# Performance work log

Measured on AMD Instinct MI355X. Metric: run time of the kernel, lower is better.

Reference implementation:

```python
import jax, jax.numpy as jnp
import numpy as np

T, S, B, H, NH, F = 256, 128, 32, 1024, 16, 4096
D = H // NH  # head dim


def setup_inputs() -> dict:
    key = jax.random.key(0)
    ks = jax.random.split(key, 14)
    w = lambda k, shape: jax.random.normal(k, shape, jnp.float32) * 0.02
    return {
        "x": jax.random.normal(ks[0], (T, B, H), jnp.float32),
        "src_bias": jnp.zeros((B, 1, 1, S), jnp.float32),
        "tgt_bias": jnp.zeros((B, 1, 1, T), jnp.float32),
        "memory": jax.random.normal(ks[1], (S, B, H), jnp.float32),
        # cross-attention projections
        "Wq": w(ks[2], (H, H)), "bq": jnp.zeros((H,), jnp.float32),
        "Wk": w(ks[3], (H, H)), "bk": jnp.zeros((H,), jnp.float32),
        "Wv": w(ks[4], (H, H)), "bv": jnp.zeros((H,), jnp.float32),
        "Wo": w(ks[5], (H, H)), "bo": jnp.zeros((H,), jnp.float32),
        # feed-forward
        "W1": w(ks[6], (H, F)), "b1": jnp.zeros((F,), jnp.float32),
        "W2": w(ks[7], (F, H)), "b2": jnp.zeros((H,), jnp.float32),
        # LSTM gates: input = cat(ffn_x, attn_ctx, h) -> 3H, output 4H (i,j,f,o)
        "Wg": w(ks[8], (3 * H, 4 * H)), "bg": jnp.zeros((4 * H,), jnp.float32),
    }


def _cross_attention(xq, mem, bias, Wq, bq, Wk, bk, Wv, bv, Wo, bo):
    # xq: [B,T,H], mem: [B,S,H], bias: [B,1,1,S]
    b, t, h = xq.shape
    q = (xq @ Wq + bq).reshape(b, t, NH, D) * (D ** -0.5)
    k = (mem @ Wk + bk).reshape(b, -1, NH, D)
    v = (mem @ Wv + bv).reshape(b, -1, NH, D)
    logits = jnp.einsum("bqhd,bkhd->bhqk", q, k) + bias
    wts = jax.nn.softmax(logits, axis=-1)
    ctx = jnp.einsum("bhqk,bkhd->bqhd", wts, v).reshape(b, t, h)
    return ctx @ Wo + bo


def reference(x, src_bias, tgt_bias, memory, Wq, bq, Wk, bk, Wv, bv, Wo, bo,
              W1, b1, W2, b2, Wg, bg):
    # cross attention (time-major -> batch-major -> time-major)
    c_attn = _cross_attention(jnp.transpose(x, (1, 0, 2)),
                              jnp.transpose(memory, (1, 0, 2)),
                              src_bias, Wq, bq, Wk, bk, Wv, bv, Wo, bo)
    c_attn = jnp.transpose(c_attn, (1, 0, 2))  # [T,B,H]

    # feed-forward on x (dropout disabled / eval mode)
    ffn_x = jax.nn.relu(x @ W1 + b1) @ W2 + b2  # [T,B,H]

    xs = jnp.concatenate([ffn_x, c_attn], axis=-1)  # [T,B,2H]
    c0 = jnp.zeros((x.shape[1], H), x.dtype)
    h0 = jnp.zeros((x.shape[1], H), x.dtype)

    def step(carry, xt):
        c, h = carry
        g = jnp.concatenate([xt, h], axis=-1) @ Wg + bg  # [B,4H]
        i = jax.nn.sigmoid(g[:, :H])
        j = jnp.tanh(g[:, H:2 * H])
        f = jax.nn.sigmoid(g[:, 2 * H:3 * H])
        o = jax.nn.sigmoid(g[:, 3 * H:])
        new_c = f * c + i * j
        new_h = o * new_c  # THUMT LSTMCell default activation=None
        return (new_c, new_h), new_h

    (c_f, h_f), hiddens = jax.lax.scan(step, (c0, h0), xs)
    return hiddens, c_f, h_f
```

## Files before the change

### kernel.cpp

```cpp
#include <hip/hip_runtime.h>
#include <cstdint>
#include <cstddef>

#define T_  256
#define S_  128
#define B_  32
#define H_  1024
#define NH_ 16
#define D_  64
#define F_  4096
#define TB_ (T_*B_)
#define SB_ (S_*B_)

typedef unsigned short u16;
typedef unsigned int   u32;
typedef unsigned long long u64;
typedef __attribute__((ext_vector_type(8))) short s16x8;
typedef __attribute__((ext_vector_type(4))) float f32x4;
typedef __attribute__((ext_vector_type(4))) u32  u32x4;

static __device__ __forceinline__ float b2f(u16 u) {
  union { u32 i; float f; } cv; cv.i = ((u32)u) << 16; return cv.f;
}
static __device__ __forceinline__ u16 f2b(float f) {
  union { float f; u32 i; } cv; cv.f = f;
  u32 u = cv.i;
  u32 r = (u + 0x7fffu + ((u >> 16) & 1u)) >> 16;
  return (u16)r;
}
static __device__ __forceinline__ float sigm(float x) {
  return 1.0f / (1.0f + __expf(-x));
}
static __device__ __forceinline__ float tanh_fast(float x) {
  float e2 = __expf(2.0f * x);
  return 1.0f - 2.0f / (e2 + 1.0f);
}

typedef const __attribute__((address_space(1))) void* gvoidp;
typedef __attribute__((address_space(3))) void* lvoidp;
static __device__ __forceinline__ void gl_lds16(const void* g, void* l) {
  __builtin_amdgcn_global_load_lds((gvoidp)g, (lvoidp)l, 16, 0, 0);
}

__global__ void cast_bf16(const float* __restrict__ in, u16* __restrict__ out, int n4) {
  int i = blockIdx.x * 256 + threadIdx.x;
  if (i < n4) {
    float4 v = reinterpret_cast<const float4*>(in)[i];
    ushort4 o;
    o.x = f2b(v.x); o.y = f2b(v.y); o.z = f2b(v.z); o.w = f2b(v.w);
    reinterpret_cast<ushort4*>(out)[i] = o;
  }
}

__global__ void transpose_cast(const float* __restrict__ in, u16* __restrict__ out,
                               int R, int C) {
  __shared__ float tile[32][33];
  int c0 = blockIdx.x * 32, r0 = blockIdx.y * 32;
  int tx = threadIdx.x, ty = threadIdx.y;
  #pragma unroll
  for (int k = 0; k < 32; k += 8)
    tile[ty + k][tx] = in[(size_t)(r0 + ty + k) * C + c0 + tx];
  __syncthreads();
  #pragma unroll
  for (int k = 0; k < 32; k += 8)
    out[(size_t)(c0 + ty + k) * R + r0 + tx] = f2b(tile[tx][ty + k]);
}

__global__ void rearrange_wh(const u16* __restrict__ WhT, u16* __restrict__ WhR) {
  int idx = blockIdx.x * 256 + threadIdx.x;
  int lane = idx & 63;
  int kc = (idx >> 6) & 7;
  int g  = (idx >> 9) & 3;
  int w  = (idx >> 11) & 3;
  int bk = idx >> 13;
  int row = g * H_ + bk * 16 + (lane & 15);
  int col = w * 256 + kc * 32 + (lane >> 4) * 8;
  *(uint4*)&WhR[(size_t)idx * 8] = *(const uint4*)&WhT[(size_t)row * H_ + col];
}

__global__ __launch_bounds__(256) void gemm_bt(
    const u16* __restrict__ A, const u16* __restrict__ Bt,
    u16* __restrict__ Out, const float* __restrict__ bias,
    int Kdim, int ostride, float scale, int relu)
{
  __shared__ __align__(16) u16 As[128 * 32];
  __shared__ __align__(16) u16 Bs[128 * 32];
  const int tid  = threadIdx.x;
  const int wave = tid >> 6, lane = tid & 63;
  const int quad = lane >> 4, l16 = lane & 15;
  const int bm = blockIdx.y << 7, bn = blockIdx.x << 7;
  const int wm = (wave & 1) << 6, wn = (wave >> 1) << 6;
  f32x4 acc[4][4] = {};

  const int sr = wave * 32 + (lane >> 2);
  const int sc = (lane & 3) * 8;
  const u16* ga = &A [(size_t)(bm + sr) * Kdim + sc];
  const u16* gb = &Bt[(size_t)(bn + sr) * Kdim + sc];
  u16* lA = &As[wave * 1024];
  u16* lB = &Bs[wave * 1024];
  const size_t rowskip = (size_t)16 * Kdim;

  for (int k0 = 0; k0 < Kdim; k0 += 32) {
    gl_lds16(ga + k0,           lA);
    gl_lds16(ga + k0 + rowskip, lA + 512);
    gl_lds16(gb + k0,           lB);
    gl_lds16(gb + k0 + rowskip, lB + 512);
    __syncthreads();
    s16x8 af[4], bf[4];
    #pragma unroll
    for (int mt = 0; mt < 4; mt++)
      af[mt] = *(const s16x8*)&As[(wm + mt * 16 + l16) * 32 + quad * 8];
    #pragma unroll
    for (int nt = 0; nt < 4; nt++)
      bf[nt] = *(const s16x8*)&Bs[(wn + nt * 16 + l16) * 32 + quad * 8];
    #pragma unroll
    for (int mt = 0; mt < 4; mt++)
      #pragma unroll
      for (int nt = 0; nt < 4; nt++)
        acc[mt][nt] = __builtin_amdgcn_mfma_f32_16x16x32_bf16(af[mt], bf[nt], acc[mt][nt], 0, 0, 0);
    __syncthreads();
  }

  #pragma unroll
  for (int mt = 0; mt < 4; mt++) {
    #pragma unroll
    for (int nt = 0; nt < 4; nt++) {
      const int col = bn + wn + nt * 16 + l16;
      const float bv = bias[col];
      #pragma unroll
      for (int r = 0; r < 4; r++) {
        const int row = bm + wm + mt * 16 + quad * 4 + r;
        float vv = (acc[mt][nt][r] + bv) * scale;
        if (relu) vv = fmaxf(vv, 0.0f);
        Out[(size_t)row * ostride + col] = f2b(vv);
      }
    }
  }
}

__global__ __launch_bounds__(256) void attn_kernel(
    const u16* __restrict__ q, const u16* __restrict__ k, const u16* __restrict__ v,
    const float* __restrict__ src_bias, u16* __restrict__ ctx)
{
  __shared__ u16 ks[S_ * D_];
  __shared__ u16 vs[S_ * D_];
  const int b  = blockIdx.x >> 4;
  const int nh = blockIdx.x & 15;
  const int tid = threadIdx.x;

  for (int i = tid; i < (S_ * D_) / 8; i += 256) {
    int s = i >> 3, c = (i & 7) * 8;
    *(uint4*)&ks[s * D_ + c] = *(const uint4*)&k[((size_t)(s * B_ + b)) * H_ + nh * D_ + c];
    *(uint4*)&vs[s * D_ + c] = *(const uint4*)&v[((size_t)(s * B_ + b)) * H_ + nh * D_ + c];
  }
  __syncthreads();

  const int t = tid;
  float qf[D_];
  const u16* qp = &q[((size_t)(t * B_ + b)) * H_ + nh * D_];
  #pragma unroll
  for (int c8 = 0; c8 < D_; c8 += 8) {
    uint4 qv = *(const uint4*)&qp[c8];
    const u16* pu = (const u16*)&qv;
    #pragma unroll
    for (int j = 0; j < 8; j++) qf[c8 + j] = b2f(pu[j]);
  }
  const float* bias = src_bias + b * S_;

  float m = -1e30f, l = 0.0f;
  for (int s = 0; s < S_; s++) {
    float dot = 0.0f;
    #pragma unroll
    for (int d = 0; d < D_; d++) dot += qf[d] * b2f(ks[s * D_ + d]);
    dot += bias[s];
    float nm = fmaxf(m, dot);
    l = l * __expf(m - nm) + __expf(dot - nm);
    m = nm;
  }
  float of[D_] = {};
  const float inv = 1.0f / l;
  for (int s = 0; s < S_; s++) {
    float dot = 0.0f;
    #pragma unroll
    for (int d = 0; d < D_; d++) dot += qf[d] * b2f(ks[s * D_ + d]);
    dot += bias[s];
    float w = __expf(dot - m) * inv;
    #pragma unroll
    for (int d = 0; d < D_; d++) of[d] += w * b2f(vs[s * D_ + d]);
  }
  u16* op = &ctx[((size_t)(t * B_ + b)) * H_ + nh * D_];
  #pragma unroll
  for (int c8 = 0; c8 < D_; c8 += 8) {
    u16 tmp[8];
    #pragma unroll
    for (int j = 0; j < 8; j++) tmp[j] = f2b(of[c8 + j]);
    *(uint4*)&op[c8] = *(const uint4*)tmp;
  }
}

#define ISSUE2(K) { \
  const u16* b0_ = hb + ((size_t)(wave * 16 + (K) * 2 + (quad >> 1))) * 512 + \
                   (quad & 1) * 8 + l16 * 16; \
  asm volatile("global_load_dwordx4 %0, %1, off sc0 sc1" : "=v"(ba[K][0]) : "v"(b0_) : "memory"); \
  asm volatile("global_load_dwordx4 %0, %1, off sc0 sc1" : "=v"(ba[K][1]) : "v"(b0_ + 256) : "memory"); }

#define DO_MFMA(A0,A1,KC)                                                           \
  { _Pragma("unroll") for (int g_ = 0; g_ < 3; g_++) {                              \
      s16x8 wf_ = *(const s16x8*)&Wl[wave][((g_ * 8 + (KC)) * 64 + lane) * 8];      \
      acc[g_][0] = __builtin_amdgcn_mfma_f32_16x16x32_bf16(A0, wf_, acc[g_][0], 0, 0, 0); \
      acc[g_][1] = __builtin_amdgcn_mfma_f32_16x16x32_bf16(A1, wf_, acc[g_][1], 0, 0, 0); } \
    acc[3][0] = __builtin_amdgcn_mfma_f32_16x16x32_bf16(A0, wo[KC], acc[3][0], 0, 0, 0);  \
    acc[3][1] = __builtin_amdgcn_mfma_f32_16x16x32_bf16(A1, wo[KC], acc[3][1], 0, 0, 0); }

#define CONSUME(K, NSTR) { \
  asm volatile("s_waitcnt vmcnt(" NSTR ")" ::: "memory"); \
  __builtin_amdgcn_sched_barrier(0); \
  DO_MFMA(ba[K][0], ba[K][1], K); }

__global__ __launch_bounds__(256, 1) void lstm_persistent(
    const u16* __restrict__ g_x, const u16* __restrict__ WhR,
    u16* __restrict__ hb16, u32* __restrict__ sent, float* __restrict__ out)
{
  __shared__ __align__(16) u16 Wl[4][3 * 8 * 64 * 8];
  __shared__ float P[4][4][32][17];
  const int bk = blockIdx.x, tid = threadIdx.x;
  const int wave = tid >> 6, lane = tid & 63;
  const int quad = lane >> 4, l16 = lane & 15;

  const u16* wsrc = WhR + ((size_t)(bk * 4 + wave) * 4 * 8 * 64) * 8;
  for (int i = lane; i < 3 * 8 * 64; i += 64)
    *(uint4*)&Wl[wave][i * 8] = *(const uint4*)&wsrc[(size_t)i * 8];
  s16x8 wo[8];
  #pragma unroll
  for (int kc = 0; kc < 8; kc++)
    wo[kc] = *(const s16x8*)&wsrc[((size_t)(3 * 8 + kc) * 64 + lane) * 8];
  __syncthreads();

  const int pb = tid >> 4, pc = tid & 15;
  const int col = bk * 16 + pc;
  float creg[2] = {0.0f, 0.0f};

  float gxp[2][4];
  #pragma unroll
  for (int ii = 0; ii < 2; ii++)
    #pragma unroll
    for (int g = 0; g < 4; g++)
      gxp[ii][g] = b2f(g_x[((size_t)(pb + ii * 16)) * (4 * H_) + g * H_ + col]);

  s16x8 ba[8][2];

  for (int t = 0; t < T_; t++) {
    if (t > 0) {
      const u32 st = (u32)t;
      const u16* hb = hb16 + ((t & 1) ^ 1) * 32768;

      { const u32* sp = sent + ((size_t)(((t & 1) ^ 1) * 256 + wave * 64 + lane));
        u32 sv;
        do {
          asm volatile("global_load_dword %0, %1, off sc0 sc1\n\ts_waitcnt vmcnt(0)"
                       : "=v"(sv) : "v"(sp) : "memory");
        } while (!__all(sv == st)); }

      f32x4 acc[4][2] = {};
      ISSUE2(0) ISSUE2(1) ISSUE2(2) ISSUE2(3)
      ISSUE2(4) ISSUE2(5) ISSUE2(6) ISSUE2(7)
      CONSUME(0, "14") CONSUME(1, "12") CONSUME(2, "10") CONSUME(3, "8")
      CONSUME(4, "6")  CONSUME(5, "4")  CONSUME(6, "2")  CONSUME(7, "0")

      #pragma unroll
      for (int g = 0; g < 4; g++)
        #pragma unroll
        for (int mt = 0; mt < 2; mt++)
          #pragma unroll
          for (int r = 0; r < 4; r++)
            P[wave][g][mt * 16 + quad * 4 + r][l16] = acc[g][mt][r];
    }
    __syncthreads();

    float gs[2][4];
    #pragma unroll
    for (int ii = 0; ii < 2; ii++) {
      const int b_ = pb + ii * 16;
      #pragma unroll
      for (int g = 0; g < 4; g++) {
        float s = gxp[ii][g];
        if (t > 0) s += P[0][g][b_][pc] + P[1][g][b_][pc] + P[2][g][b_][pc] + P[3][g][b_][pc];
        gs[ii][g] = s;
      }
    }
    __syncthreads();

    float hn[2], cn[2];
    #pragma unroll
    for (int ii = 0; ii < 2; ii++) {
      const float iv = sigm(gs[ii][0]);
      const float jv = tanh_fast(gs[ii][1]);
      const float fv = sigm(gs[ii][2]);
      const float ov = sigm(gs[ii][3]);
      cn[ii] = fv * creg[ii] + iv * jv;
      hn[ii] = ov * cn[ii];
      creg[ii] = cn[ii];
    }

    {
      u32 lo0 = f2b(hn[0]), lo1 = f2b(hn[1]);
      u32 hi0 = __shfl_down(lo0, 1), hi1 = __shfl_down(lo1, 1);
      if ((pc & 1) == 0) {
        u32* hw32 = (u32*)(hb16 + (t & 1) * 32768);
        u32 dw0 = lo0 | (hi0 << 16);
        u32 dw1 = lo1 | (hi1 << 16);
        __hip_atomic_store(&hw32[(size_t)bk * 256 + pb * 8 + (pc >> 1)], dw0,
                           __ATOMIC_RELAXED, __HIP_MEMORY_SCOPE_AGENT);
        __hip_atomic_store(&hw32[(size_t)bk * 256 + (pb + 16) * 8 + (pc >> 1)], dw1,
                           __ATOMIC_RELAXED, __HIP_MEMORY_SCOPE_AGENT);
      }
      asm volatile("s_waitcnt vmcnt(0)" ::: "memory");
      if (lane == 0)
        __hip_atomic_store(&sent[(size_t)(t & 1) * 256 + bk * 4 + wave], (u32)(t + 1),
                           __ATOMIC_RELAXED, __HIP_MEMORY_SCOPE_AGENT);
    }

    #pragma unroll
    for (int ii = 0; ii < 2; ii++) {
      const int b_ = pb + ii * 16;
      out[(size_t)t * (B_ * H_) + b_ * H_ + col] = hn[ii];
      if (t == T_ - 1) {
        out[(size_t)T_ * B_ * H_ + b_ * H_ + col] = cn[ii];
        out[(size_t)T_ * B_ * H_ + B_ * H_ + b_ * H_ + col] = hn[ii];
      }
    }
    if (t < T_ - 1) {
      #pragma unroll
      for (int ii = 0; ii < 2; ii++)
        #pragma unroll
        for (int g = 0; g < 4; g++)
          gxp[ii][g] = b2f(g_x[((size_t)(t + 1) * B_ + pb + ii * 16) * (4 * H_) + g * H_ + col]);
    }
  }
}

extern "C" void kernel_launch(void* const* d_in, const int* in_sizes, int n_in,
                              void* d_out, int out_size, void* d_ws, size_t ws_size,
                              hipStream_t stream)
{
  const float* x        = (const float*)d_in[0];
  const float* src_bias = (const float*)d_in[1];
  const float* mem      = (const float*)d_in[3];
  const float* Wq = (const float*)d_in[4];  const float* bq = (const float*)d_in[5];
  const float* Wk = (const float*)d_in[6];  const float* bk = (const float*)d_in[7];
  const float* Wv = (const float*)d_in[8];  const float* bv = (const float*)d_in[9];
  const float* Wo = (const float*)d_in[10]; const float* bo = (const float*)d_in[11];
  const float* W1 = (const float*)d_in[12]; const float* b1 = (const float*)d_in[13];
  const float* W2 = (const float*)d_in[14]; const float* b2 = (const float*)d_in[15];
  const float* Wg = (const float*)d_in[16]; const float* bg = (const float*)d_in[17];
  float* out = (float*)d_out;

  char* p = (char*)d_ws;
  u16* xb   = (u16*)p; p += (size_t)TB_ * H_ * 2;
  u16* memb = (u16*)p; p += (size_t)SB_ * H_ * 2;
  u16* WqT  = (u16*)p; p += (size_t)H_ * H_ * 2;
  u16* WkT  = (u16*)p; p += (size_t)H_ * H_ * 2;
  u16* WvT  = (u16*)p; p += (size_t)H_ * H_ * 2;
  u16* WoT  = (u16*)p; p += (size_t)H_ * H_ * 2;
  u16* W1T  = (u16*)p; p += (size_t)F_ * H_ * 2;
  u16* W2T  = (u16*)p; p += (size_t)H_ * F_ * 2;
  u16* WgxT = (u16*)p; p += (size_t)(4 * H_) * (2 * H_) * 2;
  u16* WhT  = (u16*)p; p += (size_t)(4 * H_) * H_ * 2;
  u16* WhR  = (u16*)p; p += (size_t)(4 * H_) * H_ * 2;
  u16* qb   = (u16*)p; p += (size_t)TB_ * H_ * 2;
  u16* kb   = (u16*)p; p += (size_t)SB_ * H_ * 2;
  u16* vb   = (u16*)p; p += (size_t)SB_ * H_ * 2;
  u16* ctxb = (u16*)p; p += (size_t)TB_ * H_ * 2;
  u16* xs   = (u16*)p; p += (size_t)TB_ * (2 * H_) * 2;
  u16* h1   = (u16*)p; p += (size_t)TB_ * F_ * 2;
  u16* hb16 = (u16*)p; p += (size_t)2 * 32768 * 2;
  u32* sent = (u32*)p; p += (size_t)2 * 256 * 4;
  u16* gx   = h1;

  hipMemsetAsync(sent, 0, 2 * 256 * 4, stream);

  cast_bf16<<<dim3((TB_ * H_ / 4) / 256), dim3(256), 0, stream>>>(x, xb, TB_ * H_ / 4);
  cast_bf16<<<dim3((SB_ * H_ / 4) / 256), dim3(256), 0, stream>>>(mem, memb, SB_ * H_ / 4);

  dim3 tb(32, 8);
  transpose_cast<<<dim3(H_ / 32, H_ / 32), tb, 0, stream>>>(Wq, WqT, H_, H_);
  transpose_cast<<<dim3(H_ / 32, H_ / 32), tb, 0, stream>>>(Wk, WkT, H_, H_);
  transpose_cast<<<dim3(H_ / 32, H_ / 32), tb, 0, stream>>>(Wv, WvT, H_, H_);
  transpose_cast<<<dim3(H_ / 32, H_ / 32), tb, 0, stream>>>(Wo, WoT, H_, H_);
  transpose_cast<<<dim3(F_ / 32, H_ / 32), tb, 0, stream>>>(W1, W1T, H_, F_);
  transpose_cast<<<dim3(H_ / 32, F_ / 32), tb, 0, stream>>>(W2, W2T, F_, H_);
  transpose_cast<<<dim3(4 * H_ / 32, 2 * H_ / 32), tb, 0, stream>>>(Wg, WgxT, 2 * H_, 4 * H_);
  transpose_cast<<<dim3(4 * H_ / 32, H_ / 32), tb, 0, stream>>>(Wg + (size_t)(2 * H_) * (4 * H_), WhT, H_, 4 * H_);
  rearrange_wh<<<dim3(2048), 256, 0, stream>>>(WhT, WhR);

  gemm_bt<<<dim3(H_ / 128, TB_ / 128), 256, 0, stream>>>(xb, WqT, qb, bq, H_, H_, 0.125f, 0);
  gemm_bt<<<dim3(H_ / 128, SB_ / 128), 256, 0, stream>>>(memb, WkT, kb, bk, H_, H_, 1.0f, 0);
  gemm_bt<<<dim3(H_ / 128, SB_ / 128), 256, 0, stream>>>(memb, WvT, vb, bv, H_, H_, 1.0f, 0);

  attn_kernel<<<dim3(B_ * NH_), 256, 0, stream>>>(qb, kb, vb, src_bias, ctxb);

  gemm_bt<<<dim3(H_ / 128, TB_ / 128), 256, 0, stream>>>(ctxb, WoT, xs + H_, bo, H_, 2 * H_, 1.0f, 0);

  gemm_bt<<<dim3(F_ / 128, TB_ / 128), 256, 0, stream>>>(xb, W1T, h1, b1, H_, F_, 1.0f, 1);
  gemm_bt<<<dim3(H_ / 128, TB_ / 128), 256, 0, stream>>>(h1, W2T, xs, b2, F_, 2 * H_, 1.0f, 0);

  gemm_bt<<<dim3(4 * H_ / 128, TB_ / 128), 256, 0, stream>>>(xs, WgxT, gx, bg, 2 * H_, 4 * H_, 1.0f, 0);

  lstm_persistent<<<dim3(64), 256, 0, stream>>>(gx, WhR, hb16, sent, out);
}
```

Before: 1.774 ms.

## Merge prep kernels and batch independent GEMMs into grouped launches

```diff
diff --git a/kernel.cpp b/kernel.cpp
--- a/kernel.cpp
+++ b/kernel.cpp
@@ -42,21 +42,23 @@
   __builtin_amdgcn_global_load_lds((gvoidp)g, (lvoidp)l, 16, 0, 0);
 }
 
-__global__ void cast_bf16(const float* __restrict__ in, u16* __restrict__ out, int n4) {
-  int i = blockIdx.x * 256 + threadIdx.x;
-  if (i < n4) {
-    float4 v = reinterpret_cast<const float4*>(in)[i];
-    ushort4 o;
-    o.x = f2b(v.x); o.y = f2b(v.y); o.z = f2b(v.z); o.w = f2b(v.w);
-    reinterpret_cast<ushort4*>(out)[i] = o;
-  }
-}
-
-__global__ void transpose_cast(const float* __restrict__ in, u16* __restrict__ out,
-                               int R, int C) {
-  __shared__ float tile[32][33];
-  int c0 = blockIdx.x * 32, r0 = blockIdx.y * 32;
-  int tx = threadIdx.x, ty = threadIdx.y;
+static __device__ __forceinline__ void cast_task(const float* __restrict__ in,
+                                                 u16* __restrict__ out, int lb, int tid) {
+  int i = lb * 256 + tid;
+  float4 v = reinterpret_cast<const float4*>(in)[i];
+  ushort4 o;
+  o.x = f2b(v.x); o.y = f2b(v.y); o.z = f2b(v.z); o.w = f2b(v.w);
+  reinterpret_cast<ushort4*>(out)[i] = o;
+}
+
+static __device__ __forceinline__ void tr32(const float* __restrict__ in,
+                                            u16* __restrict__ out,
+                                            int R, int C, int lin, int tid,
+                                            float tile[32][33]) {
+  const int gx = C >> 5;
+  const int bx = lin % gx, by = lin / gx;
+  const int c0 = bx << 5, r0 = by << 5;
+  const int tx = tid & 31, ty = tid >> 5;
   #pragma unroll
   for (int k = 0; k < 32; k += 8)
     tile[ty + k][tx] = in[(size_t)(r0 + ty + k) * C + c0 + tx];
@@ -66,29 +68,54 @@
     out[(size_t)(c0 + ty + k) * R + r0 + tx] = f2b(tile[tx][ty + k]);
 }
 
-__global__ void rearrange_wh(const u16* __restrict__ WhT, u16* __restrict__ WhR) {
-  int idx = blockIdx.x * 256 + threadIdx.x;
-  int lane = idx & 63;
-  int kc = (idx >> 6) & 7;
-  int g  = (idx >> 9) & 3;
-  int w  = (idx >> 11) & 3;
-  int bk = idx >> 13;
-  int row = g * H_ + bk * 16 + (lane & 15);
-  int col = w * 256 + kc * 32 + (lane >> 4) * 8;
-  *(uint4*)&WhR[(size_t)idx * 8] = *(const uint4*)&WhT[(size_t)row * H_ + col];
-}
-
-__global__ __launch_bounds__(256) void gemm_bt(
+#define NB_SENT 1
+#define NB_CX   8192
+#define NB_CM   4096
+#define NB_TSQ  1024
+#define NB_TW1  4096
+#define NB_TW2  4096
+#define NB_TGX  8192
+#define NB_TWH  4096
+#define NB_PREP (NB_SENT + NB_CX + NB_CM + 4*NB_TSQ + NB_TW1 + NB_TW2 + NB_TGX + NB_TWH)
+
+__global__ __launch_bounds__(256) void prep_all(
+    const float* __restrict__ x, const float* __restrict__ mem,
+    const float* __restrict__ Wq, const float* __restrict__ Wk,
+    const float* __restrict__ Wv, const float* __restrict__ Wo,
+    const float* __restrict__ W1, const float* __restrict__ W2,
+    const float* __restrict__ Wg,
+    u16* __restrict__ xb, u16* __restrict__ memb,
+    u16* __restrict__ WqT, u16* __restrict__ WkT, u16* __restrict__ WvT,
+    u16* __restrict__ WoT, u16* __restrict__ W1T, u16* __restrict__ W2T,
+    u16* __restrict__ WgxT, u16* __restrict__ WhT, u32* __restrict__ sent)
+{
+  __shared__ float tile[32][33];
+  int b = blockIdx.x;
+  const int tid = threadIdx.x;
+  if (b < NB_SENT) { sent[tid] = 0; sent[tid + 256] = 0; return; }
+  b -= NB_SENT;
+  if (b < NB_CX) { cast_task(x, xb, b, tid); return; }      b -= NB_CX;
+  if (b < NB_CM) { cast_task(mem, memb, b, tid); return; }  b -= NB_CM;
+  if (b < NB_TSQ) { tr32(Wq, WqT, H_, H_, b, tid, tile); return; }  b -= NB_TSQ;
+  if (b < NB_TSQ) { tr32(Wk, WkT, H_, H_, b, tid, tile); return; }  b -= NB_TSQ;
+  if (b < NB_TSQ) { tr32(Wv, WvT, H_, H_, b, tid, tile); return; }  b -= NB_TSQ;
+  if (b < NB_TSQ) { tr32(Wo, WoT, H_, H_, b, tid, tile); return; }  b -= NB_TSQ;
+  if (b < NB_TW1) { tr32(W1, W1T, H_, F_, b, tid, tile); return; }  b -= NB_TW1;
+  if (b < NB_TW2) { tr32(W2, W2T, F_, H_, b, tid, tile); return; }  b -= NB_TW2;
+  if (b < NB_TGX) { tr32(Wg, WgxT, 2 * H_, 4 * H_, b, tid, tile); return; } b -= NB_TGX;
+  tr32(Wg + (size_t)(2 * H_) * (4 * H_), WhT, H_, 4 * H_, b, tid, tile);
+}
+
+static __device__ __forceinline__ void gemm_core(
     const u16* __restrict__ A, const u16* __restrict__ Bt,
     u16* __restrict__ Out, const float* __restrict__ bias,
-    int Kdim, int ostride, float scale, int relu)
-{
-  __shared__ __align__(16) u16 As[128 * 32];
-  __shared__ __align__(16) u16 Bs[128 * 32];
+    int Kdim, int ostride, float scale, int relu,
+    int bx, int by, u16* As, u16* Bs)
+{
   const int tid  = threadIdx.x;
   const int wave = tid >> 6, lane = tid & 63;
   const int quad = lane >> 4, l16 = lane & 15;
-  const int bm = blockIdx.y << 7, bn = blockIdx.x << 7;
+  const int bm = by << 7, bn = bx << 7;
   const int wm = (wave & 1) << 6, wn = (wave >> 1) << 6;
   f32x4 acc[4][4] = {};
 
@@ -138,6 +165,28 @@
   }
 }
 
+struct GJob {
+  const u16* A; const u16* Bt; u16* Out; const float* bias;
+  int Kdim; int ostride; int relu; int gridx; int nblk; float scale;
+};
+struct GBatch { GJob j[4]; int starts[4]; int njobs; };
+
+__global__ __launch_bounds__(256) void gemm_multi(GBatch gb)
+{
+  __shared__ __align__(16) u16 As[128 * 32];
+  __shared__ __align__(16) u16 Bs[128 * 32];
+  const int bid = blockIdx.x;
+  int ji = 0;
+  #pragma unroll
+  for (int t = 1; t < 4; t++)
+    if (t < gb.njobs && bid >= gb.starts[t]) ji = t;
+  const GJob J = gb.j[ji];
+  const int lin = bid - gb.starts[ji];
+  const int wg = (lin & 7) * (J.nblk >> 3) + (lin >> 3);
+  const int bx = wg % J.gridx, by = wg / J.gridx;
+  gemm_core(J.A, J.Bt, J.Out, J.bias, J.Kdim, J.ostride, J.scale, J.relu, bx, by, As, Bs);
+}
+
 __global__ __launch_bounds__(256) void attn_kernel(
     const u16* __restrict__ q, const u16* __restrict__ k, const u16* __restrict__ v,
     const float* __restrict__ src_bias, u16* __restrict__ ctx)
@@ -218,7 +267,7 @@
   DO_MFMA(ba[K][0], ba[K][1], K); }
 
 __global__ __launch_bounds__(256, 1) void lstm_persistent(
-    const u16* __restrict__ g_x, const u16* __restrict__ WhR,
+    const u16* __restrict__ g_x, const u16* __restrict__ WhT,
     u16* __restrict__ hb16, u32* __restrict__ sent, float* __restrict__ out)
 {
   __shared__ __align__(16) u16 Wl[4][3 * 8 * 64 * 8];
@@ -227,13 +276,21 @@
   const int wave = tid >> 6, lane = tid & 63;
   const int quad = lane >> 4, l16 = lane & 15;
 
-  const u16* wsrc = WhR + ((size_t)(bk * 4 + wave) * 4 * 8 * 64) * 8;
-  for (int i = lane; i < 3 * 8 * 64; i += 64)
-    *(uint4*)&Wl[wave][i * 8] = *(const uint4*)&wsrc[(size_t)i * 8];
+  for (int i = lane; i < 3 * 8 * 64; i += 64) {
+    const int g  = (i >> 9) & 3;
+    const int kc = (i >> 6) & 7;
+    const int row = g * H_ + bk * 16 + (lane & 15);
+    const int col = wave * 256 + kc * 32 + (lane >> 4) * 8;
+    *(uint4*)&Wl[wave][i * 8] = *(const uint4*)&WhT[(size_t)row * H_ + col];
+  }
   s16x8 wo[8];
-  #pragma unroll
-  for (int kc = 0; kc < 8; kc++)
-    wo[kc] = *(const s16x8*)&wsrc[((size_t)(3 * 8 + kc) * 64 + lane) * 8];
+  {
+    const int row = 3 * H_ + bk * 16 + (lane & 15);
+    const int colb = wave * 256 + (lane >> 4) * 8;
+    #pragma unroll
+    for (int kc = 0; kc < 8; kc++)
+      wo[kc] = *(const s16x8*)&WhT[(size_t)row * H_ + colb + kc * 32];
+  }
   __syncthreads();
 
   const int pb = tid >> 4, pc = tid & 15;
@@ -350,8 +407,8 @@
   const float* Wk = (const float*)d_in[6];  const float* bk = (const float*)d_in[7];
   const float* Wv = (const float*)d_in[8];  const float* bv = (const float*)d_in[9];
   const float* Wo = (const float*)d_in[10]; const float* bo = (const float*)d_in[11];
-  const float* W1 = (const float*)d_in[12]; const float* b1 = (const float*)d_in[13];
-  const float* W2 = (const float*)d_in[14]; const float* b2 = (const float*)d_in[15];
+  const float* W1 = (const float*)d_in[12]; const float* b1f = (const float*)d_in[13];
+  const float* W2 = (const float*)d_in[14]; const float* b2f_ = (const float*)d_in[15];
   const float* Wg = (const float*)d_in[16]; const float* bg = (const float*)d_in[17];
   float* out = (float*)d_out;
 
@@ -366,7 +423,6 @@
   u16* W2T  = (u16*)p; p += (size_t)H_ * F_ * 2;
   u16* WgxT = (u16*)p; p += (size_t)(4 * H_) * (2 * H_) * 2;
   u16* WhT  = (u16*)p; p += (size_t)(4 * H_) * H_ * 2;
-  u16* WhR  = (u16*)p; p += (size_t)(4 * H_) * H_ * 2;
   u16* qb   = (u16*)p; p += (size_t)TB_ * H_ * 2;
   u16* kb   = (u16*)p; p += (size_t)SB_ * H_ * 2;
   u16* vb   = (u16*)p; p += (size_t)SB_ * H_ * 2;
@@ -377,34 +433,39 @@
   u32* sent = (u32*)p; p += (size_t)2 * 256 * 4;
   u16* gx   = h1;
 
-  hipMemsetAsync(sent, 0, 2 * 256 * 4, stream);
-
-  cast_bf16<<<dim3((TB_ * H_ / 4) / 256), dim3(256), 0, stream>>>(x, xb, TB_ * H_ / 4);
-  cast_bf16<<<dim3((SB_ * H_ / 4) / 256), dim3(256), 0, stream>>>(mem, memb, SB_ * H_ / 4);
-
-  dim3 tb(32, 8);
-  transpose_cast<<<dim3(H_ / 32, H_ / 32), tb, 0, stream>>>(Wq, WqT, H_, H_);
-  transpose_cast<<<dim3(H_ / 32, H_ / 32), tb, 0, stream>>>(Wk, WkT, H_, H_);
-  transpose_cast<<<dim3(H_ / 32, H_ / 32), tb, 0, stream>>>(Wv, WvT, H_, H_);
-  transpose_cast<<<dim3(H_ / 32, H_ / 32), tb, 0, stream>>>(Wo, WoT, H_, H_);
-  transpose_cast<<<dim3(F_ / 32, H_ / 32), tb, 0, stream>>>(W1, W1T, H_, F_);
-  transpose_cast<<<dim3(H_ / 32, F_ / 32), tb, 0, stream>>>(W2, W2T, F_, H_);
-  transpose_cast<<<dim3(4 * H_ / 32, 2 * H_ / 32), tb, 0, stream>>>(Wg, WgxT, 2 * H_, 4 * H_);
-  transpose_cast<<<dim3(4 * H_ / 32, H_ / 32), tb, 0, stream>>>(Wg + (size_t)(2 * H_) * (4 * H_), WhT, H_, 4 * H_);
-  rearrange_wh<<<dim3(2048), 256, 0, stream>>>(WhT, WhR);
-
-  gemm_bt<<<dim3(H_ / 128, TB_ / 128), 256, 0, stream>>>(xb, WqT, qb, bq, H_, H_, 0.125f, 0);
-  gemm_bt<<<dim3(H_ / 128, SB_ / 128), 256, 0, stream>>>(memb, WkT, kb, bk, H_, H_, 1.0f, 0);
-  gemm_bt<<<dim3(H_ / 128, SB_ / 128), 256, 0, stream>>>(memb, WvT, vb, bv, H_, H_, 1.0f, 0);
-
-  attn_kernel<<<dim3(B_ * NH_), 256, 0, stream>>>(qb, kb, vb, src_bias, ctxb);
-
-  gemm_bt<<<dim3(H_ / 128, TB_ / 128), 256, 0, stream>>>(ctxb, WoT, xs + H_, bo, H_, 2 * H_, 1.0f, 0);
-
-  gemm_bt<<<dim3(F_ / 128, TB_ / 128), 256, 0, stream>>>(xb, W1T, h1, b1, H_, F_, 1.0f, 1);
-  gemm_bt<<<dim3(H_ / 128, TB_ / 128), 256, 0, stream>>>(h1, W2T, xs, b2, F_, 2 * H_, 1.0f, 0);
-
-  gemm_bt<<<dim3(4 * H_ / 128, TB_ / 128), 256, 0, stream>>>(xs, WgxT, gx, bg, 2 * H_, 4 * H_, 1.0f, 0);
-
-  lstm_persistent<<<dim3(64), 256, 0, stream>>>(gx, WhR, hb16, sent, out);
-}
+  prep_all<<<dim3(NB_PREP), dim3(256), 0, stream>>>(
+      x, mem, Wq, Wk, Wv, Wo, W1, W2, Wg,
+      xb, memb, WqT, WkT, WvT, WoT, W1T, W2T, WgxT, WhT, sent);
+
+  GBatch gb1 = {};
+  gb1.j[0] = { xb,   WqT, qb, bq,  H_,     H_,     0,  H_ / 128,     TB_ / 128 * (H_ / 128),      0.125f };
+  gb1.j[1] = { memb, WkT, kb, bk,  H_,     H_,     0,  H_ / 128,     SB_ / 128 * (H_ / 128),      1.0f   };
+  gb1.j[2] = { memb, WvT, vb, bv,  H_,     H_,     0,  H_ / 128,     SB_ / 128 * (H_ / 128),      1.0f   };
+  gb1.j[3] = { xb,   W1T, h1, b1f, H_,     F_,     1,  F_ / 128,     TB_ / 128 * (F_ / 128),      1.0f   };
+  gb1.starts[0] = 0;
+  gb1.starts[1] = gb1.j[0].nblk;
+  gb1.starts[2] = gb1.starts[1] + gb1.j[1].nblk;
+  gb1.starts[3] = gb1.starts[2] + gb1.j[2].nblk;
+  gb1.njobs = 4;
+  const int nb1 = gb1.starts[3] + gb1.j[3].nblk;
+  gemm_multi<<<dim3(nb1), dim3(256), 0, stream>>>(gb1);
+
+  attn_kernel<<<dim3(B_ * NH_), dim3(256), 0, stream>>>(qb, kb, vb, src_bias, ctxb);
+
+  GBatch gb2 = {};
+  gb2.j[0] = { ctxb, WoT, xs + H_, bo,   H_, 2 * H_, 0, H_ / 128, TB_ / 128 * (H_ / 128), 1.0f };
+  gb2.j[1] = { h1,   W2T, xs,      b2f_, F_, 2 * H_, 0, H_ / 128, TB_ / 128 * (H_ / 128), 1.0f };
+  gb2.starts[0] = 0;
+  gb2.starts[1] = gb2.j[0].nblk;
+  gb2.njobs = 2;
+  const int nb2 = gb2.starts[1] + gb2.j[1].nblk;
+  gemm_multi<<<dim3(nb2), dim3(256), 0, stream>>>(gb2);
+
+  GBatch gb3 = {};
+  gb3.j[0] = { xs, WgxT, gx, bg, 2 * H_, 4 * H_, 0, 4 * H_ / 128, TB_ / 128 * (4 * H_ / 128), 1.0f };
+  gb3.starts[0] = 0;
+  gb3.njobs = 1;
+  gemm_multi<<<dim3(gb3.j[0].nblk), dim3(256), 0, stream>>>(gb3);
+
+  lstm_persistent<<<dim3(64), dim3(256), 0, stream>>>(gx, WhT, hb16, sent, out);
+}
```

Measured after the change: 1.697 ms. 1.05x faster.
